# Kernel optimization log

Hardware: AMD Instinct MI355X
Metric: run time of the kernel (lower is better)

## Reference

```python
import jax, jax.numpy as jnp
import numpy as np

B, S, DIM = 2, 1024, 1024
E, K, INTER = 16, 2, 512
SHARED_INTER = 2 * INTER  # n_shared_experts * moe_inter_dim
ROUTE_SCALE = 1.0


def setup_inputs() -> dict:
    key = jax.random.key(0)
    ks = jax.random.split(key, 8)
    init = lambda k, shape: jax.random.normal(k, shape, dtype=jnp.float32) * 0.02
    return {
        "x": jax.random.normal(ks[0], (B, S, DIM), dtype=jnp.float32),
        "gate_w": init(ks[1], (E, DIM)),
        "w1": init(ks[2], (E, INTER, DIM)),
        "w2": init(ks[3], (E, DIM, INTER)),
        "w3": init(ks[4], (E, INTER, DIM)),
        "sw1": init(ks[5], (SHARED_INTER, DIM)),
        "sw2": init(ks[6], (DIM, SHARED_INTER)),
        "sw3": init(ks[7], (SHARED_INTER, DIM)),
    }


def reference(x, gate_w, w1, w2, w3, sw1, sw2, sw3):
    b, s, d = x.shape
    xt = x.reshape(-1, d)            # [T, D] flattened tokens
    T = xt.shape[0]

    # Gate: sigmoid scores, top-k experts, normalize selected weights
    scores = jax.nn.sigmoid(xt @ gate_w.T)           # [T, E]
    topv, topi = jax.lax.top_k(scores, K)            # [T, K]
    weights = topv / jnp.sum(topv, axis=-1, keepdims=True) * ROUTE_SCALE

    # Per-token dense combine weights over experts: gate[t, e]
    gate = jnp.zeros((T, E), xt.dtype).at[jnp.arange(T)[:, None], topi].add(weights)

    # Routed experts (SwiGLU), computed densely and combined with gate weights
    h = jax.nn.silu(jnp.einsum('td,eid->tei', xt, w1)) * jnp.einsum('td,eid->tei', xt, w3)
    expert_out = jnp.einsum('tei,edi->ted', h, w2)   # [T, E, D]
    y = jnp.einsum('ted,te->td', expert_out, gate)   # [T, D]

    # Shared expert (SwiGLU MLP over all tokens)
    z = (jax.nn.silu(xt @ sw1.T) * (xt @ sw3.T)) @ sw2.T

    return (y + z).reshape(b, s, d)
```

## Files before the change

kernel.cpp:

```cpp
#include <hip/hip_runtime.h>
#include <stdint.h>

typedef unsigned short u16;
typedef __bf16 bf16x8 __attribute__((ext_vector_type(8)));
typedef float f32x4 __attribute__((ext_vector_type(4)));
typedef unsigned short u16x8 __attribute__((ext_vector_type(8)));

#define TTOK 2048
#define DIMSZ 1024
#define NROUT 16
#define INTERSZ 512
#define BK 128
#define CHK 16

__device__ __forceinline__ u16 f2bf(float f) {
    unsigned int u = __builtin_bit_cast(unsigned int, f);
    unsigned int r = u + 0x7FFFu + ((u >> 16) & 1u);
    return (u16)(r >> 16);
}

__device__ __forceinline__ void gl2lds16(const void* g, void* l) {
    __builtin_amdgcn_global_load_lds(
        (const __attribute__((address_space(1))) void*)(uintptr_t)g,
        (__attribute__((address_space(3))) void*)(uintptr_t)l,
        16, 0, 0);
}

#define NF4A (NROUT * INTERSZ * DIMSZ / 4)
#define NF4B (DIMSZ * DIMSZ / 4)
#define CASTA_BLKS 1024
#define CAST_BLKS 1152
__global__ __launch_bounds__(256) void prep(
    const float* __restrict__ w1, const float* __restrict__ sw1,
    const float* __restrict__ w3, const float* __restrict__ sw3,
    const float* __restrict__ w2, const float* __restrict__ sw2,
    u16* __restrict__ W1b, u16* __restrict__ W3b, u16* __restrict__ W2b,
    const float* __restrict__ x, const float* __restrict__ gw,
    int* __restrict__ topi, float2* __restrict__ topw,
    u16* __restrict__ Xbf, float* __restrict__ out) {
    const int r = blockIdx.y;
    const int tid = threadIdx.x;
    if (r < 3) {
        if (blockIdx.x >= CAST_BLKS) return;
        const float* a; const float* b; u16* d;
        if (r == 0)      { a = w1; b = sw1; d = W1b; }
        else if (r == 1) { a = w3; b = sw3; d = W3b; }
        else             { a = w2; b = sw2; d = W2b; }
        const float4* src = (blockIdx.x < CASTA_BLKS)
                            ? (const float4*)a
                            : (const float4*)b - (size_t)CASTA_BLKS * 2048;
        ushort4* dst = (ushort4*)d;
        const size_t gbase = (size_t)blockIdx.x * 2048;
        float4 v[8];
        #pragma unroll
        for (int k = 0; k < 8; ++k)
            v[k] = src[gbase + k * 256 + tid];
        #pragma unroll
        for (int k = 0; k < 8; ++k) {
            ushort4 o;
            o.x = f2bf(v[k].x); o.y = f2bf(v[k].y);
            o.z = f2bf(v[k].z); o.w = f2bf(v[k].w);
            dst[gbase + k * 256 + tid] = o;
        }
        return;
    }
    const int t = blockIdx.x;
    const int wave = tid >> 6, lane = tid & 63;
    const int d0 = tid * 4;
    *(float4*)(out + (size_t)t * DIMSZ + d0) = make_float4(0.f, 0.f, 0.f, 0.f);
    float4 xv = *(const float4*)(x + (size_t)t * DIMSZ + d0);
    ushort4 o;
    o.x = f2bf(xv.x); o.y = f2bf(xv.y); o.z = f2bf(xv.z); o.w = f2bf(xv.w);
    *(ushort4*)&Xbf[(size_t)t * DIMSZ + d0] = o;

    float acc[16];
    #pragma unroll
    for (int e = 0; e < 16; ++e) {
        float4 g = *(const float4*)(gw + e * DIMSZ + d0);
        acc[e] = xv.x * g.x + xv.y * g.y + xv.z * g.z + xv.w * g.w;
    }
    #pragma unroll
    for (int off = 32; off > 0; off >>= 1) {
        #pragma unroll
        for (int e = 0; e < 16; ++e) acc[e] += __shfl_xor(acc[e], off);
    }
    __shared__ float part[4][16];
    __shared__ float sfin[16];
    if (lane < 16) part[wave][lane] = acc[lane];
    __syncthreads();
    if (wave == 0 && lane < 16) {
        float s = part[0][lane] + part[1][lane] + part[2][lane] + part[3][lane];
        sfin[lane] = 1.f / (1.f + expf(-s));
    }
    __syncthreads();
    if (tid == 0) {
        int i0 = 0; float v0 = sfin[0];
        #pragma unroll
        for (int e = 1; e < 16; ++e) { float v = sfin[e]; if (v > v0) { v0 = v; i0 = e; } }
        int i1 = -1; float v1 = -1e30f;
        #pragma unroll
        for (int e = 0; e < 16; ++e) { float v = sfin[e]; if (e != i0 && v > v1) { v1 = v; i1 = e; } }
        float inv = 1.f / (v0 + v1);
        topi[t] = i0 | (i1 << 8);
        topw[t] = make_float2(v0 * inv, v1 * inv);
    }
}

__global__ __launch_bounds__(256) void route_kernel(
    const int* __restrict__ topi, const float2* __restrict__ topw,
    int* __restrict__ counts, int* __restrict__ tokidx, float* __restrict__ tokw) {
    const int e = blockIdx.x;
    const int tid = threadIdx.x;
    int p[8]; int m[8]; int cnt = 0;
    #pragma unroll
    for (int j = 0; j < 8; ++j) {
        int t = tid * 8 + j;
        p[j] = topi[t];
        m[j] = ((p[j] & 255) == e) || ((p[j] >> 8) == e) ? 1 : 0;
        cnt += m[j];
    }
    const int lane = tid & 63, wave = tid >> 6;
    int v = cnt;
    #pragma unroll
    for (int off = 1; off < 64; off <<= 1) {
        int u = __shfl_up(v, off);
        if (lane >= off) v += u;
    }
    __shared__ int wsum[4];
    if (lane == 63) wsum[wave] = v;
    __syncthreads();
    int wbase = 0;
    #pragma unroll
    for (int w = 0; w < 4; ++w) wbase += (w < wave) ? wsum[w] : 0;
    int base = wbase + v - cnt;
    #pragma unroll
    for (int j = 0; j < 8; ++j) {
        if (m[j]) {
            int t = tid * 8 + j;
            float2 w2 = topw[t];
            tokidx[e * TTOK + base] = t;
            tokw[e * TTOK + base] = ((p[j] & 255) == e) ? w2.x : w2.y;
            ++base;
        }
    }
    if (tid == 0) counts[e] = wsum[0] + wsum[1] + wsum[2] + wsum[3];
}

__global__ __launch_bounds__(256) void gemm1s(
    const u16* __restrict__ Xbf, const u16* __restrict__ W1b,
    const u16* __restrict__ W3b, const int* __restrict__ counts,
    const int* __restrict__ tokidx, const float* __restrict__ tokw,
    u16* __restrict__ Hc, u16* __restrict__ Hs) {
    const int e = blockIdx.z;
    const int cnt = (e < NROUT) ? counts[e] : TTOK;
    const int m0 = blockIdx.y * 64;
    if (m0 >= cnt) return;
    const int n0 = blockIdx.x * 64;
    __shared__ u16 As[64 * BK], B1s[64 * BK], B3s[64 * BK];
    const u16* B1 = W1b + ((size_t)e * INTERSZ + n0) * DIMSZ;
    const u16* B3 = W3b + ((size_t)e * INTERSZ + n0) * DIMSZ;
    const int tid = threadIdx.x;

    int row[4], cgs[4]; size_t arow[4];
    #pragma unroll
    for (int i = 0; i < 4; ++i) {
        int c = tid + i * 256;
        row[i] = c >> 4;
        cgs[i] = ((c & 15) ^ (row[i] & 7)) * 8;
        int slot = m0 + row[i];
        int g;
        if (e < NROUT) g = (slot < cnt) ? tokidx[e * TTOK + slot] : 0;
        else           g = slot;
        arow[i] = (size_t)g * DIMSZ;
    }
    f32x4 acc1[2][2] = {}; f32x4 acc3[2][2] = {};
    const int wave = tid >> 6, lane = tid & 63;
    const int wm = (wave >> 1) * 32, wn = (wave & 1) * 32;
    const int lr = lane & 15, lq = lane >> 4;

    for (int kt = 0; kt < DIMSZ / BK; ++kt) {
        const int k0 = kt * BK;
        #pragma unroll
        for (int i = 0; i < 4; ++i) {
            int c = tid + i * 256;
            gl2lds16(Xbf + arow[i] + k0 + cgs[i], &As[c * 8]);
            size_t boff = (size_t)row[i] * DIMSZ + k0 + cgs[i];
            gl2lds16(B1 + boff, &B1s[c * 8]);
            gl2lds16(B3 + boff, &B3s[c * 8]);
        }
        __syncthreads();
        #pragma unroll
        for (int ks = 0; ks < 4; ++ks) {
            bf16x8 af[2], b1f[2], b3f[2];
            const int g = ks * 4 + lq;
            #pragma unroll
            for (int mt = 0; mt < 2; ++mt) {
                int m = wm + mt * 16 + lr;
                af[mt] = *(const bf16x8*)&As[(m * CHK + (g ^ (m & 7))) * 8];
            }
            #pragma unroll
            for (int nt = 0; nt < 2; ++nt) {
                int n = wn + nt * 16 + lr;
                int ch = (n * CHK + (g ^ (n & 7))) * 8;
                b1f[nt] = *(const bf16x8*)&B1s[ch];
                b3f[nt] = *(const bf16x8*)&B3s[ch];
            }
            #pragma unroll
            for (int mt = 0; mt < 2; ++mt) {
                #pragma unroll
                for (int nt = 0; nt < 2; ++nt) {
                    acc1[mt][nt] = __builtin_amdgcn_mfma_f32_16x16x32_bf16(af[mt], b1f[nt], acc1[mt][nt], 0, 0, 0);
                    acc3[mt][nt] = __builtin_amdgcn_mfma_f32_16x16x32_bf16(af[mt], b3f[nt], acc3[mt][nt], 0, 0, 0);
                }
            }
        }
        __syncthreads();
    }
    #pragma unroll
    for (int mt = 0; mt < 2; ++mt) {
        #pragma unroll
        for (int nt = 0; nt < 2; ++nt) {
            #pragma unroll
            for (int r = 0; r < 4; ++r) {
                int m = wm + mt * 16 + lq * 4 + r;
                int n = wn + nt * 16 + lr;
                int slot = m0 + m;
                bool valid = slot < cnt;
                float h1 = acc1[mt][nt][r], h3 = acc3[mt][nt][r];
                float hv = 0.f;
                if (valid) {
                    float tw = (e < NROUT) ? tokw[e * TTOK + slot] : 1.0f;
                    hv = h1 / (1.f + __expf(-h1)) * h3 * tw;
                }
                if (e < NROUT)
                    Hc[((size_t)e * TTOK + slot) * INTERSZ + n0 + n] = f2bf(hv);
                else
                    Hs[(size_t)slot * DIMSZ + (e - NROUT) * INTERSZ + n0 + n] = f2bf(hv);
            }
        }
    }
}

__global__ __launch_bounds__(256) void gemm2u(
    const u16* __restrict__ Hc, const u16* __restrict__ Hs,
    const u16* __restrict__ W2b, const u16* __restrict__ W2sb,
    const int* __restrict__ counts, const int* __restrict__ tokidx,
    float* __restrict__ out) {
    const int e = blockIdx.z;
    const bool routed = (e < NROUT);
    const int cnt = routed ? counts[e] : TTOK;
    const int m0 = blockIdx.y * 64;
    if (m0 >= cnt) return;
    const int n0 = blockIdx.x * 64;
    const int klen = routed ? INTERSZ : DIMSZ;
    __shared__ u16 As[64 * BK], Bs[64 * BK];
    const u16* A0 = routed ? Hc + ((size_t)e * TTOK + m0) * INTERSZ
                           : Hs + (size_t)m0 * DIMSZ;
    const u16* B0 = routed ? W2b + ((size_t)e * DIMSZ + n0) * INTERSZ
                           : W2sb + (size_t)n0 * DIMSZ;
    const int tid = threadIdx.x;
    const int wave = tid >> 6, lane = tid & 63;
    const int wm = (wave >> 1) * 32, wn = (wave & 1) * 32;
    const int lr = lane & 15, lq = lane >> 4;

    int row[4], cgs[4];
    #pragma unroll
    for (int i = 0; i < 4; ++i) {
        int c = tid + i * 256;
        row[i] = c >> 4;
        cgs[i] = ((c & 15) ^ (row[i] & 7)) * 8;
    }

    f32x4 acc[2][2] = {};
    for (int kt = 0; kt < klen / BK; ++kt) {
        const int k0 = kt * BK;
        #pragma unroll
        for (int i = 0; i < 4; ++i) {
            int c = tid + i * 256;
            gl2lds16(A0 + (size_t)row[i] * klen + k0 + cgs[i], &As[c * 8]);
            gl2lds16(B0 + (size_t)row[i] * klen + k0 + cgs[i], &Bs[c * 8]);
        }
        __syncthreads();
        #pragma unroll
        for (int ks = 0; ks < 4; ++ks) {
            bf16x8 af[2], bfr[2];
            const int g = ks * 4 + lq;
            #pragma unroll
            for (int mt = 0; mt < 2; ++mt) {
                int m = wm + mt * 16 + lr;
                af[mt] = *(const bf16x8*)&As[(m * CHK + (g ^ (m & 7))) * 8];
            }
            #pragma unroll
            for (int nt = 0; nt < 2; ++nt) {
                int n = wn + nt * 16 + lr;
                bfr[nt] = *(const bf16x8*)&Bs[(n * CHK + (g ^ (n & 7))) * 8];
            }
            #pragma unroll
            for (int mt = 0; mt < 2; ++mt) {
                #pragma unroll
                for (int nt = 0; nt < 2; ++nt) {
                    acc[mt][nt] = __builtin_amdgcn_mfma_f32_16x16x32_bf16(af[mt], bfr[nt], acc[mt][nt], 0, 0, 0);
                }
            }
        }
        __syncthreads();
    }
    #pragma unroll
    for (int mt = 0; mt < 2; ++mt) {
        #pragma unroll
        for (int r = 0; r < 4; ++r) {
            int m = wm + mt * 16 + lq * 4 + r;
            int slot = m0 + m;
            if (slot < cnt) {
                int t = routed ? tokidx[e * TTOK + slot] : slot;
                #pragma unroll
                for (int nt = 0; nt < 2; ++nt) {
                    int n = wn + nt * 16 + lr;
                    unsafeAtomicAdd(&out[(size_t)t * DIMSZ + n0 + n], acc[mt][nt][r]);
                }
            }
        }
    }
}

extern "C" void kernel_launch(void* const* d_in, const int* in_sizes, int n_in,
                              void* d_out, int out_size, void* d_ws, size_t ws_size,
                              hipStream_t stream) {
    const float* x      = (const float*)d_in[0];
    const float* gate_w = (const float*)d_in[1];
    const float* w1     = (const float*)d_in[2];
    const float* w2     = (const float*)d_in[3];
    const float* w3     = (const float*)d_in[4];
    const float* sw1    = (const float*)d_in[5];
    const float* sw2    = (const float*)d_in[6];
    const float* sw3    = (const float*)d_in[7];
    float* out = (float*)d_out;

    char* ws = (char*)d_ws;
    const size_t SZ_W   = (size_t)(NROUT + 2) * INTERSZ * DIMSZ * 2;
    const size_t SZ_XBF = (size_t)TTOK * DIMSZ * 2;
    u16*   W1b    = (u16*)(ws);
    u16*   W3b    = (u16*)(ws + SZ_W);
    u16*   W2all  = (u16*)(ws + 2 * SZ_W);
    u16*   Xbf    = (u16*)(ws + 3 * SZ_W);
    char*  route  = ws + 3 * SZ_W + SZ_XBF;
    int*   counts = (int*)route;
    int*   topi   = (int*)(route + 256);
    float2* topw  = (float2*)(route + 256 + TTOK * 4);
    int*   tokidx = (int*)(route + 256 + TTOK * 12);
    float* tokw   = (float*)(route + 256 + TTOK * 12 + 16 * TTOK * 4);
    char*  hbuf   = route + 256 + TTOK * 12 + 2 * (size_t)16 * TTOK * 4;
    u16*   Hc     = (u16*)hbuf;
    u16*   Hs     = (u16*)(hbuf + (size_t)NROUT * TTOK * INTERSZ * 2);
    u16*   W2sb   = W2all + (size_t)NROUT * DIMSZ * INTERSZ;

    prep<<<dim3(2048, 4), 256, 0, stream>>>(
        w1, sw1, w3, sw3, w2, sw2, W1b, W3b, W2all,
        x, gate_w, topi, topw, Xbf, out);
    route_kernel<<<NROUT, 256, 0, stream>>>(topi, topw, counts, tokidx, tokw);
    gemm1s<<<dim3(INTERSZ / 64, TTOK / 64, NROUT + 2), 256, 0, stream>>>(
        Xbf, W1b, W3b, counts, tokidx, tokw, Hc, Hs);
    gemm2u<<<dim3(DIMSZ / 64, TTOK / 64, NROUT + 1), 256, 0, stream>>>(
        Hc, Hs, W2all, W2sb, counts, tokidx, out);
}
```

Measured before the change: 233.5 us.

## Replace atomic output accumulation with per-slot buffers combined in shared-expert GEMM

The routed down-projection now writes each token's expert contribution with plain stores into one of two fp32 buffers, chosen by whether the expert is the token's first or second top-k pick. A separate shared-expert GEMM then computes its result and sums it with both buffers into the output. This removes the zeroing of the output in prep and all float atomics on the output. In exchange it adds a second kernel launch, reads and writes two extra 8 MB buffers, and serialises the shared-expert work after the routed work. It assumes the packed topi entry encodes the first expert in its low byte.

```diff
diff --git a/kernel.cpp b/kernel.cpp
--- a/kernel.cpp
+++ b/kernel.cpp
@@ -37,7 +37,7 @@
     u16* __restrict__ W1b, u16* __restrict__ W3b, u16* __restrict__ W2b,
     const float* __restrict__ x, const float* __restrict__ gw,
     int* __restrict__ topi, float2* __restrict__ topw,
-    u16* __restrict__ Xbf, float* __restrict__ out) {
+    u16* __restrict__ Xbf) {
     const int r = blockIdx.y;
     const int tid = threadIdx.x;
     if (r < 3) {
@@ -67,7 +67,6 @@
     const int t = blockIdx.x;
     const int wave = tid >> 6, lane = tid & 63;
     const int d0 = tid * 4;
-    *(float4*)(out + (size_t)t * DIMSZ + d0) = make_float4(0.f, 0.f, 0.f, 0.f);
     float4 xv = *(const float4*)(x + (size_t)t * DIMSZ + d0);
     ushort4 o;
     o.x = f2bf(xv.x); o.y = f2bf(xv.y); o.z = f2bf(xv.z); o.w = f2bf(xv.w);
@@ -241,23 +240,19 @@
     }
 }
 
-__global__ __launch_bounds__(256) void gemm2u(
-    const u16* __restrict__ Hc, const u16* __restrict__ Hs,
-    const u16* __restrict__ W2b, const u16* __restrict__ W2sb,
+__global__ __launch_bounds__(256) void gemm2rt(
+    const u16* __restrict__ Hc, const u16* __restrict__ W2b,
     const int* __restrict__ counts, const int* __restrict__ tokidx,
-    float* __restrict__ out) {
+    const int* __restrict__ topi,
+    float* __restrict__ bufA, float* __restrict__ bufB) {
     const int e = blockIdx.z;
-    const bool routed = (e < NROUT);
-    const int cnt = routed ? counts[e] : TTOK;
+    const int cnt = counts[e];
     const int m0 = blockIdx.y * 64;
     if (m0 >= cnt) return;
     const int n0 = blockIdx.x * 64;
-    const int klen = routed ? INTERSZ : DIMSZ;
     __shared__ u16 As[64 * BK], Bs[64 * BK];
-    const u16* A0 = routed ? Hc + ((size_t)e * TTOK + m0) * INTERSZ
-                           : Hs + (size_t)m0 * DIMSZ;
-    const u16* B0 = routed ? W2b + ((size_t)e * DIMSZ + n0) * INTERSZ
-                           : W2sb + (size_t)n0 * DIMSZ;
+    const u16* A0 = Hc + ((size_t)e * TTOK + m0) * INTERSZ;
+    const u16* B0 = W2b + ((size_t)e * DIMSZ + n0) * INTERSZ;
     const int tid = threadIdx.x;
     const int wave = tid >> 6, lane = tid & 63;
     const int wm = (wave >> 1) * 32, wn = (wave & 1) * 32;
@@ -272,13 +267,13 @@
     }
 
     f32x4 acc[2][2] = {};
-    for (int kt = 0; kt < klen / BK; ++kt) {
+    for (int kt = 0; kt < INTERSZ / BK; ++kt) {
         const int k0 = kt * BK;
         #pragma unroll
         for (int i = 0; i < 4; ++i) {
             int c = tid + i * 256;
-            gl2lds16(A0 + (size_t)row[i] * klen + k0 + cgs[i], &As[c * 8]);
-            gl2lds16(B0 + (size_t)row[i] * klen + k0 + cgs[i], &Bs[c * 8]);
+            gl2lds16(A0 + (size_t)row[i] * INTERSZ + k0 + cgs[i], &As[c * 8]);
+            gl2lds16(B0 + (size_t)row[i] * INTERSZ + k0 + cgs[i], &Bs[c * 8]);
         }
         __syncthreads();
         #pragma unroll
@@ -312,12 +307,84 @@
             int m = wm + mt * 16 + lq * 4 + r;
             int slot = m0 + m;
             if (slot < cnt) {
-                int t = routed ? tokidx[e * TTOK + slot] : slot;
+                int t = tokidx[e * TTOK + slot];
+                float* db = ((topi[t] & 255) == e) ? bufA : bufB;
                 #pragma unroll
                 for (int nt = 0; nt < 2; ++nt) {
                     int n = wn + nt * 16 + lr;
-                    unsafeAtomicAdd(&out[(size_t)t * DIMSZ + n0 + n], acc[mt][nt][r]);
+                    db[(size_t)t * DIMSZ + n0 + n] = acc[mt][nt][r];
                 }
+            }
+        }
+    }
+}
+
+__global__ __launch_bounds__(256) void gemm2sh(
+    const u16* __restrict__ Hs, const u16* __restrict__ W2sb,
+    const float* __restrict__ bufA, const float* __restrict__ bufB,
+    float* __restrict__ out) {
+    const int m0 = blockIdx.y * 64;
+    const int n0 = blockIdx.x * 64;
+    __shared__ u16 As[64 * BK], Bs[64 * BK];
+    const u16* A0 = Hs + (size_t)m0 * DIMSZ;
+    const u16* B0 = W2sb + (size_t)n0 * DIMSZ;
+    const int tid = threadIdx.x;
+    const int wave = tid >> 6, lane = tid & 63;
+    const int wm = (wave >> 1) * 32, wn = (wave & 1) * 32;
+    const int lr = lane & 15, lq = lane >> 4;
+
+    int row[4], cgs[4];
+    #pragma unroll
+    for (int i = 0; i < 4; ++i) {
+        int c = tid + i * 256;
+        row[i] = c >> 4;
+        cgs[i] = ((c & 15) ^ (row[i] & 7)) * 8;
+    }
+
+    f32x4 acc[2][2] = {};
+    for (int kt = 0; kt < DIMSZ / BK; ++kt) {
+        const int k0 = kt * BK;
+        #pragma unroll
+        for (int i = 0; i < 4; ++i) {
+            int c = tid + i * 256;
+            gl2lds16(A0 + (size_t)row[i] * DIMSZ + k0 + cgs[i], &As[c * 8]);
+            gl2lds16(B0 + (size_t)row[i] * DIMSZ + k0 + cgs[i], &Bs[c * 8]);
+        }
+        __syncthreads();
+        #pragma unroll
+        for (int ks = 0; ks < 4; ++ks) {
+            bf16x8 af[2], bfr[2];
+            const int g = ks * 4 + lq;
+            #pragma unroll
+            for (int mt = 0; mt < 2; ++mt) {
+                int m = wm + mt * 16 + lr;
+                af[mt] = *(const bf16x8*)&As[(m * CHK + (g ^ (m & 7))) * 8];
+            }
+            #pragma unroll
+            for (int nt = 0; nt < 2; ++nt) {
+                int n = wn + nt * 16 + lr;
+                bfr[nt] = *(const bf16x8*)&Bs[(n * CHK + (g ^ (n & 7))) * 8];
+            }
+            #pragma unroll
+            for (int mt = 0; mt < 2; ++mt) {
+                #pragma unroll
+                for (int nt = 0; nt < 2; ++nt) {
+                    acc[mt][nt] = __builtin_amdgcn_mfma_f32_16x16x32_bf16(af[mt], bfr[nt], acc[mt][nt], 0, 0, 0);
+                }
+            }
+        }
+        __syncthreads();
+    }
+    #pragma unroll
+    for (int mt = 0; mt < 2; ++mt) {
+        #pragma unroll
+        for (int r = 0; r < 4; ++r) {
+            int t = m0 + wm + mt * 16 + lq * 4 + r;
+            #pragma unroll
+            for (int nt = 0; nt < 2; ++nt) {
+                int n = wn + nt * 16 + lr;
+                size_t idx = (size_t)t * DIMSZ + n0 + n;
+                out[idx] = acc[mt][nt][r] + bufA[idx] + bufB[idx];
             }
         }
     }
@@ -352,14 +419,19 @@
     char*  hbuf   = route + 256 + TTOK * 12 + 2 * (size_t)16 * TTOK * 4;
     u16*   Hc     = (u16*)hbuf;
     u16*   Hs     = (u16*)(hbuf + (size_t)NROUT * TTOK * INTERSZ * 2);
+    char*  bufs   = hbuf + (size_t)NROUT * TTOK * INTERSZ * 2 + (size_t)TTOK * DIMSZ * 2;
+    float* bufA   = (float*)bufs;
+    float* bufB   = (float*)(bufs + (size_t)TTOK * DIMSZ * 4);
     u16*   W2sb   = W2all + (size_t)NROUT * DIMSZ * INTERSZ;
 
     prep<<<dim3(2048, 4), 256, 0, stream>>>(
         w1, sw1, w3, sw3, w2, sw2, W1b, W3b, W2all,
-        x, gate_w, topi, topw, Xbf, out);
+        x, gate_w, topi, topw, Xbf);
     route_kernel<<<NROUT, 256, 0, stream>>>(topi, topw, counts, tokidx, tokw);
     gemm1s<<<dim3(INTERSZ / 64, TTOK / 64, NROUT + 2), 256, 0, stream>>>(
         Xbf, W1b, W3b, counts, tokidx, tokw, Hc, Hs);
-    gemm2u<<<dim3(DIMSZ / 64, TTOK / 64, NROUT + 1), 256, 0, stream>>>(
-        Hc, Hs, W2all, W2sb, counts, tokidx, out);
-}
+    gemm2rt<<<dim3(DIMSZ / 64, TTOK / 64, NROUT), 256, 0, stream>>>(
+        Hc, W2all, counts, tokidx, topi, bufA, bufB);
+    gemm2sh<<<dim3(DIMSZ / 64, TTOK / 64), 256, 0, stream>>>(
+        Hs, W2sb, bufA, bufB, out);
+}
```

Result: no change. 230.8 us (-1.1%).
